# Kernel tuning notes

Measured on AMD Instinct MI355X. Metric: run time of the kernel, lower is better.

Reference implementation:

```python
import jax, jax.numpy as jnp
import numpy as np

E = 1024      # embed_dim
H = 16        # num_heads
HD = E // H   # head_dim = 64


def setup_inputs() -> dict:
    key = jax.random.key(0)
    ks = jax.random.split(key, 8)
    T, B, S = 1024, 4, 1024
    return {
        "query": jax.random.normal(ks[0], (T, B, E), jnp.float32),
        "key": jax.random.normal(ks[1], (S, B, E), jnp.float32),
        "value": jax.random.normal(ks[2], (S, B, E), jnp.float32),
        "attn_mask": jax.random.normal(ks[3], (T, S), jnp.float32),
        "key_padding_mask": jax.random.randint(ks[4], (B, S), 0, 2, jnp.int32),
        "in_proj_weight": jax.random.normal(ks[5], (3 * E, E), jnp.float32) * 0.02,
        "in_proj_bias": jnp.zeros((3 * E,), jnp.float32),
        "out_w": jax.random.normal(ks[6], (E, E), jnp.float32) * 0.02,
        "out_b": jnp.zeros((E,), jnp.float32),
    }


def reference(query, key, value, attn_mask, key_padding_mask,
              in_proj_weight, in_proj_bias, out_w, out_b):
    T, B, _ = query.shape
    S = key.shape[0]
    w_q, w_k, w_v = jnp.split(in_proj_weight, 3, axis=0)   # each [E, E]
    b_q, b_k, b_v = jnp.split(in_proj_bias, 3, axis=0)
    q = query @ w_q.T + b_q                                # [T, B, E]
    k = key @ w_k.T + b_k                                  # [S, B, E]
    v = value @ w_v.T + b_v                                # [S, B, E]
    # [len, B, E] -> [B*H, len, HD]
    q = q.reshape(T, B * H, HD).transpose(1, 0, 2) / jnp.sqrt(jnp.float32(HD))
    k = k.reshape(S, B * H, HD).transpose(1, 0, 2)
    v = v.reshape(S, B * H, HD).transpose(1, 0, 2)
    scores = jnp.einsum('bth,bsh->bts', q, k)              # [B*H, T, S]
    scores = scores + attn_mask[None]                      # float additive mask
    pad = key_padding_mask.astype(bool)                    # [B, S]
    pad = jnp.broadcast_to(pad[:, None, None, :], (B, H, 1, S)).reshape(B * H, 1, S)
    scores = jnp.where(pad, -jnp.inf, scores)
    weights = jax.nn.softmax(scores, axis=-1)              # dropout p=0 -> identity
    out = jnp.einsum('bts,bsh->bth', weights, v)           # [B*H, T, HD]
    out = out.transpose(1, 0, 2).reshape(T, B, E)
    out = out @ out_w.T + out_b
    weights_avg = weights.reshape(B, H, T, S).mean(axis=1) # sum/H == mean
    return out, weights_avg
```

## Files before the change

kernel.cpp:

```cpp
#include <hip/hip_runtime.h>
#include <stdint.h>

typedef short bf16x8 __attribute__((ext_vector_type(8)));
typedef float f32x4  __attribute__((ext_vector_type(4)));

#define LOG2E_F 1.4426950408889634f
#define QSCALE_F 0.1803368801111204f

__device__ __forceinline__ unsigned short f2bf(float f) {
    unsigned int u = __float_as_uint(f);
    return (unsigned short)((u + 0x7FFFu + ((u >> 16) & 1u)) >> 16);
}

__device__ __forceinline__ unsigned short f2bfu(float f) {
    return (unsigned short)((__float_as_uint(f) + 0x8000u) >> 16);
}

__device__ __forceinline__ uint4 pack8(float4 a, float4 b) {
    union { unsigned short us[8]; uint4 v; } p;
    p.us[0] = f2bf(a.x); p.us[1] = f2bf(a.y); p.us[2] = f2bf(a.z); p.us[3] = f2bf(a.w);
    p.us[4] = f2bf(b.x); p.us[5] = f2bf(b.y); p.us[6] = f2bf(b.z); p.us[7] = f2bf(b.w);
    return p.v;
}

__global__ __launch_bounds__(256)
void cvt_kernel(const float* __restrict__ q, const float* __restrict__ k,
                const float* __restrict__ v, const float* __restrict__ w,
                const float* __restrict__ ow,
                uint4* __restrict__ Xb, uint4* __restrict__ Wb, uint4* __restrict__ OWb)
{
    const unsigned g = blockIdx.x * 256 + threadIdx.x;
    const float* src;
    uint4* dst;
    if (g < 1572864u) {
        dst = Xb + g;
        if (g < 524288u)        src = q + (size_t)g * 8;
        else if (g < 1048576u)  src = k + (size_t)(g - 524288u) * 8;
        else                    src = v + (size_t)(g - 1048576u) * 8;
    } else if (g < 1966080u) {
        src = w + (size_t)(g - 1572864u) * 8;
        dst = Wb + (g - 1572864u);
    } else {
        src = ow + (size_t)(g - 1966080u) * 8;
        dst = OWb + (g - 1966080u);
    }
    float4 a = *(const float4*)src;
    float4 b = *(const float4*)(src + 4);
    *dst = pack8(a, b);
}

__global__ __launch_bounds__(256)
void qkv_proj_kernel(const unsigned short* __restrict__ Xb, const unsigned short* __restrict__ Wb,
                     const float* __restrict__ bias,
                     unsigned short* __restrict__ Qb, unsigned short* __restrict__ Kb,
                     unsigned short* __restrict__ Vtb)
{
    const int z = blockIdx.z;
    const int j   = blockIdx.x;
    const int xcd = j & 7, idx = j >> 3;
    const int row0 = ((xcd << 2) + (idx >> 3)) * 128;
    const int col0 = (idx & 7) * 128;
    const int wofs = z << 10;

    const unsigned short* A = Xb + (size_t)z * 4194304;
    const unsigned short* B = Wb;

    __shared__ __align__(16) unsigned short As[128 * 72];
    __shared__ __align__(16) unsigned short Bs[128 * 72];

    const int tid  = threadIdx.x;
    const int lane = tid & 63;
    const int wv   = tid >> 6;
    const int wr   = wv >> 1, wc = wv & 1;

    const f32x4 zero4 = {0.f, 0.f, 0.f, 0.f};
    f32x4 acc[4][4];
#pragma unroll
    for (int m = 0; m < 4; ++m)
#pragma unroll
        for (int n = 0; n < 4; ++n) acc[m][n] = zero4;

    const int srow = tid >> 1;
    const int scol = (tid & 1) << 5;
    const int arow = wr * 64 + (lane & 15);
    const int brow = wc * 64 + (lane & 15);
    const int kof  = (lane >> 4) << 3;

    const unsigned short* pa = A + (size_t)(row0 + srow) * 1024 + scol;
    const unsigned short* pb = B + (size_t)(wofs + col0 + srow) * 1024 + scol;
    uint4 ra0 = *(const uint4*)(pa + 0),  ra1 = *(const uint4*)(pa + 8);
    uint4 ra2 = *(const uint4*)(pa + 16), ra3 = *(const uint4*)(pa + 24);
    uint4 rb0 = *(const uint4*)(pb + 0),  rb1 = *(const uint4*)(pb + 8);
    uint4 rb2 = *(const uint4*)(pb + 16), rb3 = *(const uint4*)(pb + 24);

    for (int k0 = 0; k0 < 1024; k0 += 64) {
        __syncthreads();
        *(uint4*)&As[srow * 72 + scol]      = ra0;
        *(uint4*)&As[srow * 72 + scol + 8]  = ra1;
        *(uint4*)&As[srow * 72 + scol + 16] = ra2;
        *(uint4*)&As[srow * 72 + scol + 24] = ra3;
        *(uint4*)&Bs[srow * 72 + scol]      = rb0;
        *(uint4*)&Bs[srow * 72 + scol + 8]  = rb1;
        *(uint4*)&Bs[srow * 72 + scol + 16] = rb2;
        *(uint4*)&Bs[srow * 72 + scol + 24] = rb3;
        __syncthreads();

        if (k0 < 960) {
            pa = A + (size_t)(row0 + srow) * 1024 + k0 + 64 + scol;
            pb = B + (size_t)(wofs + col0 + srow) * 1024 + k0 + 64 + scol;
            ra0 = *(const uint4*)(pa + 0);  ra1 = *(const uint4*)(pa + 8);
            ra2 = *(const uint4*)(pa + 16); ra3 = *(const uint4*)(pa + 24);
            rb0 = *(const uint4*)(pb + 0);  rb1 = *(const uint4*)(pb + 8);
            rb2 = *(const uint4*)(pb + 16); rb3 = *(const uint4*)(pb + 24);
        }

#pragma unroll
        for (int kk = 0; kk < 2; ++kk) {
            bf16x8 af[4], bfr[4];
#pragma unroll
            for (int m = 0; m < 4; ++m)
                af[m] = *(const bf16x8*)&As[(arow + m * 16) * 72 + kk * 32 + kof];
#pragma unroll
            for (int n = 0; n < 4; ++n)
                bfr[n] = *(const bf16x8*)&Bs[(brow + n * 16) * 72 + kk * 32 + kof];
#pragma unroll
            for (int m = 0; m < 4; ++m)
#pragma unroll
                for (int n = 0; n < 4; ++n)
                    acc[m][n] = __builtin_amdgcn_mfma_f32_16x16x32_bf16(af[m], bfr[n], acc[m][n], 0, 0, 0);
        }
    }

    const int ccol = lane & 15;
    const int crow = (lane >> 4) << 2;
#pragma unroll
    for (int n = 0; n < 4; ++n) {
        const int gc   = col0 + wc * 64 + n * 16 + ccol;
        const float bv = bias[wofs + gc];
        const int head = gc >> 6, d = gc & 63;
#pragma unroll
        for (int m = 0; m < 4; ++m) {
#pragma unroll
            for (int r = 0; r < 4; ++r) {
                const int gr = row0 + wr * 64 + m * 16 + crow + r;
                const int t  = gr >> 2, b = gr & 3;
                const int bh = (b << 4) + head;
                float vv = acc[m][n][r] + bv;
                if (z == 0)      Qb [((size_t)bh << 16) + ((size_t)t << 6) + d]  = f2bf(vv * QSCALE_F);
                else if (z == 1) Kb [((size_t)bh << 16) + ((size_t)t << 6) + d]  = f2bf(vv);
                else             Vtb[((size_t)bh << 16) + ((size_t)d << 10) + t] = f2bf(vv);
            }
        }
    }
}

__global__ __launch_bounds__(512)
void flash_kernel(const unsigned short* __restrict__ Qb, const unsigned short* __restrict__ Kb,
                  const unsigned short* __restrict__ Vtb, const float* __restrict__ attn_mask,
                  const int* __restrict__ padmask,
                  float* __restrict__ rl_buf, unsigned short* __restrict__ attn_out)
{
    const int j   = blockIdx.x;
    const int xcd = j & 7, idx = j >> 3;
    const int bh  = xcd * 8 + (idx >> 3);
    const int t0  = (idx & 7) << 7;
    const int b   = bh >> 4, h = bh & 15;

    __shared__ __align__(16) unsigned short Ks[2][64 * 72];
    __shared__ __align__(16) unsigned short Vs[2][64 * 72];
    __shared__ __align__(16) unsigned short Ps[128 * 72];

    const int tid  = threadIdx.x;
    const int lane = tid & 63;
    const int wv   = tid >> 6;
    const int kof  = (lane >> 4) << 3;
    const int c16  = lane & 15;

    const unsigned short* Qbase = Qb  + ((size_t)bh << 16);
    const unsigned short* Kbase = Kb  + ((size_t)bh << 16);
    const unsigned short* Vbase = Vtb + ((size_t)bh << 16);

    bf16x8 qf[2];
#pragma unroll
    for (int kk = 0; kk < 2; ++kk)
        qf[kk] = *(const bf16x8*)(Qbase + ((size_t)(t0 + wv * 16 + c16) << 6) + kk * 32 + kof);

    const bf16x8 ones = {16256, 16256, 16256, 16256, 16256, 16256, 16256, 16256};

    const f32x4 zero4 = {0.f, 0.f, 0.f, 0.f};
    f32x4 acco[4];
#pragma unroll
    for (int nd = 0; nd < 4; ++nd) acco[nd] = zero4;
    f32x4 acc_l = zero4;

    const int srow_st = tid >> 3;
    const int scol_st = (tid & 7) << 3;

    const int rbase = wv * 16 + ((lane >> 4) << 2);
    const int tr    = t0 + rbase;

    const unsigned short* kp = Kbase + ((size_t)srow_st << 6) + scol_st;
    const unsigned short* vp = Vbase + ((size_t)srow_st << 10) + scol_st;
    uint4 ka = *(const uint4*)kp;
    uint4 kb = *(const uint4*)(kp + 4096);
    uint4 va = *(const uint4*)vp;
    uint4 vb = *(const uint4*)(vp + 64);

    for (int rd = 0; rd < 8; ++rd) {
        const int s0 = rd << 7;
        __syncthreads();
        *(uint4*)&Ks[0][srow_st * 72 + scol_st] = ka;
        *(uint4*)&Ks[1][srow_st * 72 + scol_st] = kb;
        *(uint4*)&Vs[0][srow_st * 72 + scol_st] = va;
        *(uint4*)&Vs[1][srow_st * 72 + scol_st] = vb;
        __syncthreads();

        if (rd < 7) {
            const int sn = s0 + 128;
            kp = Kbase + ((size_t)(sn + srow_st) << 6) + scol_st;
            vp = Vbase + ((size_t)srow_st << 10) + sn + scol_st;
            ka = *(const uint4*)kp;
            kb = *(const uint4*)(kp + 4096);
            va = *(const uint4*)vp;
            vb = *(const uint4*)(vp + 64);
        }

        f32x4 accsA[4], accsB[4];
#pragma unroll
        for (int n = 0; n < 4; ++n) { accsA[n] = zero4; accsB[n] = zero4; }
        __builtin_amdgcn_s_setprio(1);
#pragma unroll
        for (int n = 0; n < 4; ++n) {
            bf16x8 kfA0 = *(const bf16x8*)&Ks[0][(n * 16 + c16) * 72 + kof];
            bf16x8 kfA1 = *(const bf16x8*)&Ks[0][(n * 16 + c16) * 72 + 32 + kof];
            accsA[n] = __builtin_amdgcn_mfma_f32_16x16x32_bf16(qf[0], kfA0, accsA[n], 0, 0, 0);
            accsA[n] = __builtin_amdgcn_mfma_f32_16x16x32_bf16(qf[1], kfA1, accsA[n], 0, 0, 0);
            bf16x8 kfB0 = *(const bf16x8*)&Ks[1][(n * 16 + c16) * 72 + kof];
            bf16x8 kfB1 = *(const bf16x8*)&Ks[1][(n * 16 + c16) * 72 + 32 + kof];
            accsB[n] = __builtin_amdgcn_mfma_f32_16x16x32_bf16(qf[0], kfB0, accsB[n], 0, 0, 0);
            accsB[n] = __builtin_amdgcn_mfma_f32_16x16x32_bf16(qf[1], kfB1, accsB[n], 0, 0, 0);
        }
        __builtin_amdgcn_s_setprio(0);

        int padA[4], padB[4];
#pragma unroll
        for (int n = 0; n < 4; ++n) {
            padA[n] = padmask[(b << 10) + s0 + n * 16 + c16];
            padB[n] = padmask[(b << 10) + s0 + 64 + n * 16 + c16];
        }

#pragma unroll
        for (int r = 0; r < 4; ++r) {
            const float* mp = attn_mask + (size_t)(tr + r) * 1024 + s0 + c16;
            float x0 = fmaf(mp[ 0], LOG2E_F, accsA[0][r]);
            float x1 = fmaf(mp[16], LOG2E_F, accsA[1][r]);
            float x2 = fmaf(mp[32], LOG2E_F, accsA[2][r]);
            float x3 = fmaf(mp[48], LOG2E_F, accsA[3][r]);
            if (padA[0]) x0 = -1e30f;
            if (padA[1]) x1 = -1e30f;
            if (padA[2]) x2 = -1e30f;
            if (padA[3]) x3 = -1e30f;
            const int prow = rbase + r;
            Ps[prow * 72 +  0 + c16] = f2bfu(__builtin_amdgcn_exp2f(x0));
            Ps[prow * 72 + 16 + c16] = f2bfu(__builtin_amdgcn_exp2f(x1));
            Ps[prow * 72 + 32 + c16] = f2bfu(__builtin_amdgcn_exp2f(x2));
            Ps[prow * 72 + 48 + c16] = f2bfu(__builtin_amdgcn_exp2f(x3));
        }
        __builtin_amdgcn_s_setprio(1);
#pragma unroll
        for (int kk2 = 0; kk2 < 2; ++kk2) {
            bf16x8 pf = *(const bf16x8*)&Ps[(wv * 16 + c16) * 72 + kk2 * 32 + kof];
#pragma unroll
            for (int nd = 0; nd < 4; ++nd) {
                bf16x8 vf = *(const bf16x8*)&Vs[0][(nd * 16 + c16) * 72 + kk2 * 32 + kof];
                acco[nd] = __builtin_amdgcn_mfma_f32_16x16x32_bf16(pf, vf, acco[nd], 0, 0, 0);
            }
            acc_l = __builtin_amdgcn_mfma_f32_16x16x32_bf16(pf, ones, acc_l, 0, 0, 0);
        }
        __builtin_amdgcn_s_setprio(0);

#pragma unroll
        for (int r = 0; r < 4; ++r) {
            const float* mp = attn_mask + (size_t)(tr + r) * 1024 + s0 + 64 + c16;
            float x0 = fmaf(mp[ 0], LOG2E_F, accsB[0][r]);
            float x1 = fmaf(mp[16], LOG2E_F, accsB[1][r]);
            float x2 = fmaf(mp[32], LOG2E_F, accsB[2][r]);
            float x3 = fmaf(mp[48], LOG2E_F, accsB[3][r]);
            if (padB[0]) x0 = -1e30f;
            if (padB[1]) x1 = -1e30f;
            if (padB[2]) x2 = -1e30f;
            if (padB[3]) x3 = -1e30f;
            const int prow = rbase + r;
            Ps[prow * 72 +  0 + c16] = f2bfu(__builtin_amdgcn_exp2f(x0));
            Ps[prow * 72 + 16 + c16] = f2bfu(__builtin_amdgcn_exp2f(x1));
            Ps[prow * 72 + 32 + c16] = f2bfu(__builtin_amdgcn_exp2f(x2));
            Ps[prow * 72 + 48 + c16] = f2bfu(__builtin_amdgcn_exp2f(x3));
        }
        __builtin_amdgcn_s_setprio(1);
#pragma unroll
        for (int kk2 = 0; kk2 < 2; ++kk2) {
            bf16x8 pf = *(const bf16x8*)&Ps[(wv * 16 + c16) * 72 + kk2 * 32 + kof];
#pragma unroll
            for (int nd = 0; nd < 4; ++nd) {
                bf16x8 vf = *(const bf16x8*)&Vs[1][(nd * 16 + c16) * 72 + kk2 * 32 + kof];
                acco[nd] = __builtin_amdgcn_mfma_f32_16x16x32_bf16(pf, vf, acco[nd], 0, 0, 0);
            }
            acc_l = __builtin_amdgcn_mfma_f32_16x16x32_bf16(pf, ones, acc_l, 0, 0, 0);
        }
        __builtin_amdgcn_s_setprio(0);
    }

#pragma unroll
    for (int r = 0; r < 4; ++r) {
        const int t = t0 + rbase + r;
        const float rl = 1.0f / acc_l[r];
        if (c16 == 0)
            rl_buf[(bh << 10) + t] = rl;
#pragma unroll
        for (int nd = 0; nd < 4; ++nd) {
            const int d = nd * 16 + c16;
            attn_out[((size_t)t * 4 + b) * 1024 + h * 64 + d] = f2bf(acco[nd][r] * rl);
        }
    }
}

__global__ __launch_bounds__(256)
void wavg_kernel(const unsigned short* __restrict__ Qb, const unsigned short* __restrict__ Kb,
                 const float* __restrict__ attn_mask, const int* __restrict__ padmask,
                 const float* __restrict__ rl_buf, float* __restrict__ wout)
{
    const int j   = blockIdx.x;
    const int xcd = j & 7;
    const int b   = xcd >> 1;
    const int rr  = ((j >> 3) << 1) + (xcd & 1);
    const int t0  = (rr >> 4) << 6;
    const int s0  = (rr & 15) << 6;

    __shared__ __align__(16) unsigned short Qs[64 * 72];
    __shared__ __align__(16) unsigned short Ks2[64 * 72];

    const int tid  = threadIdx.x;
    const int lane = tid & 63;
    const int wv   = tid >> 6;
    const int wr   = wv >> 1, wc = wv & 1;
    const int kof  = (lane >> 4) << 3;
    const int srow_st = tid >> 2;
    const int scol_st = (tid & 3) << 4;

    const int t_base = t0 + wr * 32 + ((lane >> 4) << 2);
    const int s_base = s0 + wc * 32 + (lane & 15);

    int pad2[2];
#pragma unroll
    for (int nn = 0; nn < 2; ++nn) pad2[nn] = padmask[(b << 10) + s_base + nn * 16];

    float maskv[2][2][4];
#pragma unroll
    for (int mm = 0; mm < 2; ++mm)
#pragma unroll
        for (int r = 0; r < 4; ++r)
#pragma unroll
            for (int nn = 0; nn < 2; ++nn)
                maskv[mm][nn][r] = attn_mask[(size_t)(t_base + mm * 16 + r) * 1024 + s_base + nn * 16] * LOG2E_F;

    float wsum[2][2][4];
#pragma unroll
    for (int mm = 0; mm < 2; ++mm)
#pragma unroll
        for (int nn = 0; nn < 2; ++nn)
#pragma unroll
            for (int r = 0; r < 4; ++r) wsum[mm][nn][r] = 0.f;

    for (int h = 0; h < 16; ++h) {
        const int bh = (b << 4) + h;
        __syncthreads();
        {
            const unsigned short* qp = Qb + ((size_t)bh << 16) + ((size_t)(t0 + srow_st) << 6) + scol_st;
            *(uint4*)&Qs[srow_st * 72 + scol_st]     = *(const uint4*)qp;
            *(uint4*)&Qs[srow_st * 72 + scol_st + 8] = *(const uint4*)(qp + 8);
            const unsigned short* kp = Kb + ((size_t)bh << 16) + ((size_t)(s0 + srow_st) << 6) + scol_st;
            *(uint4*)&Ks2[srow_st * 72 + scol_st]     = *(const uint4*)kp;
            *(uint4*)&Ks2[srow_st * 72 + scol_st + 8] = *(const uint4*)(kp + 8);
        }
        __syncthreads();

        float rlv[2][4];
#pragma unroll
        for (int mm = 0; mm < 2; ++mm)
#pragma unroll
            for (int r = 0; r < 4; ++r)
                rlv[mm][r] = rl_buf[(bh << 10) + t_base + mm * 16 + r];

        const f32x4 zero4 = {0.f, 0.f, 0.f, 0.f};
        f32x4 accs[2][2];
#pragma unroll
        for (int mm = 0; mm < 2; ++mm)
#pragma unroll
            for (int nn = 0; nn < 2; ++nn) accs[mm][nn] = zero4;
#pragma unroll
        for (int nn = 0; nn < 2; ++nn) {
            bf16x8 kf0 = *(const bf16x8*)&Ks2[(wc * 32 + nn * 16 + (lane & 15)) * 72 + kof];
            bf16x8 kf1 = *(const bf16x8*)&Ks2[(wc * 32 + nn * 16 + (lane & 15)) * 72 + 32 + kof];
#pragma unroll
            for (int mm = 0; mm < 2; ++mm) {
                bf16x8 qf0 = *(const bf16x8*)&Qs[(wr * 32 + mm * 16 + (lane & 15)) * 72 + kof];
                bf16x8 qf1 = *(const bf16x8*)&Qs[(wr * 32 + mm * 16 + (lane & 15)) * 72 + 32 + kof];
                accs[mm][nn] = __builtin_amdgcn_mfma_f32_16x16x32_bf16(qf0, kf0, accs[mm][nn], 0, 0, 0);
                accs[mm][nn] = __builtin_amdgcn_mfma_f32_16x16x32_bf16(qf1, kf1, accs[mm][nn], 0, 0, 0);
            }
        }
#pragma unroll
        for (int mm = 0; mm < 2; ++mm)
#pragma unroll
            for (int nn = 0; nn < 2; ++nn)
#pragma unroll
                for (int r = 0; r < 4; ++r)
                    if (!pad2[nn]) {
                        float x = accs[mm][nn][r] + maskv[mm][nn][r];
                        wsum[mm][nn][r] += __builtin_amdgcn_exp2f(x) * rlv[mm][r];
                    }
    }

#pragma unroll
    for (int mm = 0; mm < 2; ++mm)
#pragma unroll
        for (int nn = 0; nn < 2; ++nn)
#pragma unroll
            for (int r = 0; r < 4; ++r)
                wout[((size_t)b << 20) + (size_t)(t_base + mm * 16 + r) * 1024 + s_base + nn * 16]
                    = wsum[mm][nn][r] * 0.0625f;
}

__global__ __launch_bounds__(256)
void out_proj_kernel(const unsigned short* __restrict__ A, const unsigned short* __restrict__ Wb,
                     const float* __restrict__ bias, float* __restrict__ out)
{
    const int j   = blockIdx.x;
    const int xcd = j & 7, idx = j >> 3;
    const int row0 = ((xcd << 2) + (idx >> 3)) * 128;
    const int col0 = (idx & 7) * 128;

    __shared__ __align__(16) unsigned short As[128 * 72];
    __shared__ __align__(16) unsigned short Bs[128 * 72];

    const int tid  = threadIdx.x;
    const int lane = tid & 63;
    const int wv   = tid >> 6;
    const int wr   = wv >> 1, wc = wv & 1;

    const f32x4 zero4 = {0.f, 0.f, 0.f, 0.f};
    f32x4 acc[4][4];
#pragma unroll
    for (int m = 0; m < 4; ++m)
#pragma unroll
        for (int n = 0; n < 4; ++n) acc[m][n] = zero4;

    const int srow = tid >> 1;
    const int scol = (tid & 1) << 5;
    const int arow = wr * 64 + (lane & 15);
    const int brow = wc * 64 + (lane & 15);
    const int kof  = (lane >> 4) << 3;

    const unsigned short* pa = A  + (size_t)(row0 + srow) * 1024 + scol;
    const unsigned short* pb = Wb + (size_t)(col0 + srow) * 1024 + scol;
    uint4 ra0 = *(const uint4*)(pa + 0),  ra1 = *(const uint4*)(pa + 8);
    uint4 ra2 = *(const uint4*)(pa + 16), ra3 = *(const uint4*)(pa + 24);
    uint4 rb0 = *(const uint4*)(pb + 0),  rb1 = *(const uint4*)(pb + 8);
    uint4 rb2 = *(const uint4*)(pb + 16), rb3 = *(const uint4*)(pb + 24);

    for (int k0 = 0; k0 < 1024; k0 += 64) {
        __syncthreads();
        *(uint4*)&As[srow * 72 + scol]      = ra0;
        *(uint4*)&As[srow * 72 + scol + 8]  = ra1;
        *(uint4*)&As[srow * 72 + scol + 16] = ra2;
        *(uint4*)&As[srow * 72 + scol + 24] = ra3;
        *(uint4*)&Bs[srow * 72 + scol]      = rb0;
        *(uint4*)&Bs[srow * 72 + scol + 8]  = rb1;
        *(uint4*)&Bs[srow * 72 + scol + 16] = rb2;
        *(uint4*)&Bs[srow * 72 + scol + 24] = rb3;
        __syncthreads();

        if (k0 < 960) {
            pa = A  + (size_t)(row0 + srow) * 1024 + k0 + 64 + scol;
            pb = Wb + (size_t)(col0 + srow) * 1024 + k0 + 64 + scol;
            ra0 = *(const uint4*)(pa + 0);  ra1 = *(const uint4*)(pa + 8);
            ra2 = *(const uint4*)(pa + 16); ra3 = *(const uint4*)(pa + 24);
            rb0 = *(const uint4*)(pb + 0);  rb1 = *(const uint4*)(pb + 8);
            rb2 = *(const uint4*)(pb + 16); rb3 = *(const uint4*)(pb + 24);
        }

#pragma unroll
        for (int kk = 0; kk < 2; ++kk) {
            bf16x8 af[4], bfr[4];
#pragma unroll
            for (int m = 0; m < 4; ++m)
                af[m] = *(const bf16x8*)&As[(arow + m * 16) * 72 + kk * 32 + kof];
#pragma unroll
            for (int n = 0; n < 4; ++n)
                bfr[n] = *(const bf16x8*)&Bs[(brow + n * 16) * 72 + kk * 32 + kof];
#pragma unroll
            for (int m = 0; m < 4; ++m)
#pragma unroll
                for (int n = 0; n < 4; ++n)
                    acc[m][n] = __builtin_amdgcn_mfma_f32_16x16x32_bf16(af[m], bfr[n], acc[m][n], 0, 0, 0);
        }
    }

    const int ccol = lane & 15;
    const int crow = (lane >> 4) << 2;
#pragma unroll
    for (int n = 0; n < 4; ++n) {
        const int gc   = col0 + wc * 64 + n * 16 + ccol;
        const float bv = bias[gc];
#pragma unroll
        for (int m = 0; m < 4; ++m) {
#pragma unroll
            for (int r = 0; r < 4; ++r) {
                const int gr = row0 + wr * 64 + m * 16 + crow + r;
                out[(size_t)gr * 1024 + gc] = acc[m][n][r] + bv;
            }
        }
    }
}

extern "C" void kernel_launch(void* const* d_in, const int* in_sizes, int n_in,
                              void* d_out, int out_size, void* d_ws, size_t ws_size,
                              hipStream_t stream)
{
    const float* query     = (const float*)d_in[0];
    const float* key       = (const float*)d_in[1];
    const float* value     = (const float*)d_in[2];
    const float* attn_mask = (const float*)d_in[3];
    const int*   padmask   = (const int*)  d_in[4];
    const float* in_proj_w = (const float*)d_in[5];
    const float* in_proj_b = (const float*)d_in[6];
    const float* out_w     = (const float*)d_in[7];
    const float* out_b     = (const float*)d_in[8];

    float* out  = (float*)d_out;
    float* wavg = out + 4194304;

    char* ws = (char*)d_ws;
    unsigned short* Qb     = (unsigned short*)(ws);
    unsigned short* Kb     = (unsigned short*)(ws + 8388608);
    unsigned short* Vtb    = (unsigned short*)(ws + 16777216);
    unsigned short* Xb     = (unsigned short*)(ws + 25165824);
    unsigned short* attn_o = (unsigned short*)(ws + 25165824);
    unsigned short* Wb     = (unsigned short*)(ws + 50331648);
    unsigned short* OWb    = (unsigned short*)(ws + 56623104);
    float*          rl_buf = (float*)(ws + 58720256);

    cvt_kernel<<<dim3(8192), 256, 0, stream>>>(query, key, value, in_proj_w, out_w,
                                               (uint4*)Xb, (uint4*)Wb, (uint4*)OWb);
    qkv_proj_kernel<<<dim3(256, 1, 3), 256, 0, stream>>>(Xb, Wb, in_proj_b, Qb, Kb, Vtb);
    flash_kernel<<<dim3(512), 512, 0, stream>>>(Qb, Kb, Vtb, attn_mask, padmask,
                                                rl_buf, attn_o);
    wavg_kernel<<<dim3(1024), 256, 0, stream>>>(Qb, Kb, attn_mask, padmask,
                                                rl_buf, wavg);
    out_proj_kernel<<<dim3(256), 256, 0, stream>>>(attn_o, OWb, out_b, out);
}
```

Measured before the change: 151.9 us.

## Double-buffer shared-memory K/V and Q/K tiles in flash and weights kernels

Both the flash attention kernel and the averaged-weights kernel now keep two shared-memory buffers for their K/V (or Q/K) tiles. The next tile is written into the alternate buffer while the current one is consumed, and global loads are prefetched two iterations ahead. This cuts the two barriers per iteration down to one and gives global load latency more time to hide. In exchange it doubles LDS use in both kernels, which may lower occupancy, and it keeps more prefetch registers live.

```diff
diff --git a/kernel.cpp b/kernel.cpp
--- a/kernel.cpp
+++ b/kernel.cpp
@@ -166,8 +166,8 @@
     const int t0  = (idx & 7) << 7;
     const int b   = bh >> 4, h = bh & 15;
 
-    __shared__ __align__(16) unsigned short Ks[2][64 * 72];
-    __shared__ __align__(16) unsigned short Vs[2][64 * 72];
+    __shared__ __align__(16) unsigned short Ks[2][2][64 * 72];
+    __shared__ __align__(16) unsigned short Vs[2][2][64 * 72];
     __shared__ __align__(16) unsigned short Ps[128 * 72];
 
     const int tid  = threadIdx.x;
@@ -201,46 +201,43 @@
 
     const unsigned short* kp = Kbase + ((size_t)srow_st << 6) + scol_st;
     const unsigned short* vp = Vbase + ((size_t)srow_st << 10) + scol_st;
-    uint4 ka = *(const uint4*)kp;
-    uint4 kb = *(const uint4*)(kp + 4096);
-    uint4 va = *(const uint4*)vp;
-    uint4 vb = *(const uint4*)(vp + 64);
+    uint4 kA = *(const uint4*)kp;
+    uint4 kB = *(const uint4*)(kp + 4096);
+    uint4 vA = *(const uint4*)vp;
+    uint4 vB = *(const uint4*)(vp + 64);
+
+    *(uint4*)&Ks[0][0][srow_st * 72 + scol_st] = kA;
+    *(uint4*)&Ks[0][1][srow_st * 72 + scol_st] = kB;
+    *(uint4*)&Vs[0][0][srow_st * 72 + scol_st] = vA;
+    *(uint4*)&Vs[0][1][srow_st * 72 + scol_st] = vB;
+
+    kp = Kbase + ((size_t)(128 + srow_st) << 6) + scol_st;
+    vp = Vbase + ((size_t)srow_st << 10) + 128 + scol_st;
+    kA = *(const uint4*)kp;
+    kB = *(const uint4*)(kp + 4096);
+    vA = *(const uint4*)vp;
+    vB = *(const uint4*)(vp + 64);
+    __syncthreads();
 
     for (int rd = 0; rd < 8; ++rd) {
-        const int s0 = rd << 7;
-        __syncthreads();
-        *(uint4*)&Ks[0][srow_st * 72 + scol_st] = ka;
-        *(uint4*)&Ks[1][srow_st * 72 + scol_st] = kb;
-        *(uint4*)&Vs[0][srow_st * 72 + scol_st] = va;
-        *(uint4*)&Vs[1][srow_st * 72 + scol_st] = vb;
-        __syncthreads();
+        const int cur = rd & 1;
+        const int s0  = rd << 7;
 
         if (rd < 7) {
-            const int sn = s0 + 128;
+            *(uint4*)&Ks[cur ^ 1][0][srow_st * 72 + scol_st] = kA;
+            *(uint4*)&Ks[cur ^ 1][1][srow_st * 72 + scol_st] = kB;
+            *(uint4*)&Vs[cur ^ 1][0][srow_st * 72 + scol_st] = vA;
+            *(uint4*)&Vs[cur ^ 1][1][srow_st * 72 + scol_st] = vB;
+        }
+        if (rd < 6) {
+            const int sn = s0 + 256;
             kp = Kbase + ((size_t)(sn + srow_st) << 6) + scol_st;
             vp = Vbase + ((size_t)srow_st << 10) + sn + scol_st;
-            ka = *(const uint4*)kp;
-            kb = *(const uint4*)(kp + 4096);
-            va = *(const uint4*)vp;
-            vb = *(const uint4*)(vp + 64);
-        }
-
-        f32x4 accsA[4], accsB[4];
-#pragma unroll
-        for (int n = 0; n < 4; ++n) { accsA[n] = zero4; accsB[n] = zero4; }
-        __builtin_amdgcn_s_setprio(1);
-#pragma unroll
-        for (int n = 0; n < 4; ++n) {
-            bf16x8 kfA0 = *(const bf16x8*)&Ks[0][(n * 16 + c16) * 72 + kof];
-            bf16x8 kfA1 = *(const bf16x8*)&Ks[0][(n * 16 + c16) * 72 + 32 + kof];
-            accsA[n] = __builtin_amdgcn_mfma_f32_16x16x32_bf16(qf[0], kfA0, accsA[n], 0, 0, 0);
-            accsA[n] = __builtin_amdgcn_mfma_f32_16x16x32_bf16(qf[1], kfA1, accsA[n], 0, 0, 0);
-            bf16x8 kfB0 = *(const bf16x8*)&Ks[1][(n * 16 + c16) * 72 + kof];
-            bf16x8 kfB1 = *(const bf16x8*)&Ks[1][(n * 16 + c16) * 72 + 32 + kof];
-            accsB[n] = __builtin_amdgcn_mfma_f32_16x16x32_bf16(qf[0], kfB0, accsB[n], 0, 0, 0);
-            accsB[n] = __builtin_amdgcn_mfma_f32_16x16x32_bf16(qf[1], kfB1, accsB[n], 0, 0, 0);
-        }
-        __builtin_amdgcn_s_setprio(0);
+            kA = *(const uint4*)kp;
+            kB = *(const uint4*)(kp + 4096);
+            vA = *(const uint4*)vp;
+            vB = *(const uint4*)(vp + 64);
+        }
 
         int padA[4], padB[4];
 #pragma unroll
@@ -248,6 +245,23 @@
             padA[n] = padmask[(b << 10) + s0 + n * 16 + c16];
             padB[n] = padmask[(b << 10) + s0 + 64 + n * 16 + c16];
         }
+
+        f32x4 accsA[4], accsB[4];
+#pragma unroll
+        for (int n = 0; n < 4; ++n) { accsA[n] = zero4; accsB[n] = zero4; }
+        __builtin_amdgcn_s_setprio(1);
+#pragma unroll
+        for (int n = 0; n < 4; ++n) {
+            bf16x8 kfA0 = *(const bf16x8*)&Ks[cur][0][(n * 16 + c16) * 72 + kof];
+            bf16x8 kfA1 = *(const bf16x8*)&Ks[cur][0][(n * 16 + c16) * 72 + 32 + kof];
+            accsA[n] = __builtin_amdgcn_mfma_f32_16x16x32_bf16(qf[0], kfA0, accsA[n], 0, 0, 0);
+            accsA[n] = __builtin_amdgcn_mfma_f32_16x16x32_bf16(qf[1], kfA1, accsA[n], 0, 0, 0);
+            bf16x8 kfB0 = *(const bf16x8*)&Ks[cur][1][(n * 16 + c16) * 72 + kof];
+            bf16x8 kfB1 = *(const bf16x8*)&Ks[cur][1][(n * 16 + c16) * 72 + 32 + kof];
+            accsB[n] = __builtin_amdgcn_mfma_f32_16x16x32_bf16(qf[0], kfB0, accsB[n], 0, 0, 0);
+            accsB[n] = __builtin_amdgcn_mfma_f32_16x16x32_bf16(qf[1], kfB1, accsB[n], 0, 0, 0);
+        }
+        __builtin_amdgcn_s_setprio(0);
 
 #pragma unroll
         for (int r = 0; r < 4; ++r) {
@@ -272,7 +286,7 @@
             bf16x8 pf = *(const bf16x8*)&Ps[(wv * 16 + c16) * 72 + kk2 * 32 + kof];
 #pragma unroll
             for (int nd = 0; nd < 4; ++nd) {
-                bf16x8 vf = *(const bf16x8*)&Vs[0][(nd * 16 + c16) * 72 + kk2 * 32 + kof];
+                bf16x8 vf = *(const bf16x8*)&Vs[cur][0][(nd * 16 + c16) * 72 + kk2 * 32 + kof];
                 acco[nd] = __builtin_amdgcn_mfma_f32_16x16x32_bf16(pf, vf, acco[nd], 0, 0, 0);
             }
             acc_l = __builtin_amdgcn_mfma_f32_16x16x32_bf16(pf, ones, acc_l, 0, 0, 0);
@@ -302,12 +316,14 @@
             bf16x8 pf = *(const bf16x8*)&Ps[(wv * 16 + c16) * 72 + kk2 * 32 + kof];
 #pragma unroll
             for (int nd = 0; nd < 4; ++nd) {
-                bf16x8 vf = *(const bf16x8*)&Vs[1][(nd * 16 + c16) * 72 + kk2 * 32 + kof];
+                bf16x8 vf = *(const bf16x8*)&Vs[cur][1][(nd * 16 + c16) * 72 + kk2 * 32 + kof];
                 acco[nd] = __builtin_amdgcn_mfma_f32_16x16x32_bf16(pf, vf, acco[nd], 0, 0, 0);
             }
             acc_l = __builtin_amdgcn_mfma_f32_16x16x32_bf16(pf, ones, acc_l, 0, 0, 0);
         }
         __builtin_amdgcn_s_setprio(0);
+
+        if (rd < 7) __syncthreads();
     }
 
 #pragma unroll
@@ -336,8 +352,8 @@
     const int t0  = (rr >> 4) << 6;
     const int s0  = (rr & 15) << 6;
 
-    __shared__ __align__(16) unsigned short Qs[64 * 72];
-    __shared__ __align__(16) unsigned short Ks2[64 * 72];
+    __shared__ __align__(16) unsigned short Qs[2][64 * 72];
+    __shared__ __align__(16) unsigned short Ks2[2][64 * 72];
 
     const int tid  = threadIdx.x;
     const int lane = tid & 63;
@@ -371,18 +387,42 @@
 #pragma unroll
             for (int r = 0; r < 4; ++r) wsum[mm][nn][r] = 0.f;
 
+    const unsigned short* qsrc = Qb + ((size_t)(t0 + srow_st) << 6) + scol_st;
+    const unsigned short* ksrc = Kb + ((size_t)(s0 + srow_st) << 6) + scol_st;
+    const size_t bh0 = (size_t)(b << 4) << 16;
+
+    uint4 q0 = *(const uint4*)(qsrc + bh0);
+    uint4 q1 = *(const uint4*)(qsrc + bh0 + 8);
+    uint4 k0 = *(const uint4*)(ksrc + bh0);
+    uint4 k1 = *(const uint4*)(ksrc + bh0 + 8);
+    *(uint4*)&Qs[0][srow_st * 72 + scol_st]      = q0;
+    *(uint4*)&Qs[0][srow_st * 72 + scol_st + 8]  = q1;
+    *(uint4*)&Ks2[0][srow_st * 72 + scol_st]     = k0;
+    *(uint4*)&Ks2[0][srow_st * 72 + scol_st + 8] = k1;
+    q0 = *(const uint4*)(qsrc + bh0 + 65536);
+    q1 = *(const uint4*)(qsrc + bh0 + 65536 + 8);
+    k0 = *(const uint4*)(ksrc + bh0 + 65536);
+    k1 = *(const uint4*)(ksrc + bh0 + 65536 + 8);
+    __syncthreads();
+
+#pragma unroll 2
     for (int h = 0; h < 16; ++h) {
-        const int bh = (b << 4) + h;
-        __syncthreads();
-        {
-            const unsigned short* qp = Qb + ((size_t)bh << 16) + ((size_t)(t0 + srow_st) << 6) + scol_st;
-            *(uint4*)&Qs[srow_st * 72 + scol_st]     = *(const uint4*)qp;
-            *(uint4*)&Qs[srow_st * 72 + scol_st + 8] = *(const uint4*)(qp + 8);
-            const unsigned short* kp = Kb + ((size_t)bh << 16) + ((size_t)(s0 + srow_st) << 6) + scol_st;
-            *(uint4*)&Ks2[srow_st * 72 + scol_st]     = *(const uint4*)kp;
-            *(uint4*)&Ks2[srow_st * 72 + scol_st + 8] = *(const uint4*)(kp + 8);
-        }
-        __syncthreads();
+        const int cur = h & 1;
+        const int bh  = (b << 4) + h;
+
+        if (h < 15) {
+            *(uint4*)&Qs[cur ^ 1][srow_st * 72 + scol_st]      = q0;
+            *(uint4*)&Qs[cur ^ 1][srow_st * 72 + scol_st + 8]  = q1;
+            *(uint4*)&Ks2[cur ^ 1][srow_st * 72 + scol_st]     = k0;
+            *(uint4*)&Ks2[cur ^ 1][srow_st * 72 + scol_st + 8] = k1;
+        }
+        if (h < 14) {
+            const size_t of = bh0 + (size_t)(h + 2) * 65536;
+            q0 = *(const uint4*)(qsrc + of);
+            q1 = *(const uint4*)(qsrc + of + 8);
+            k0 = *(const uint4*)(ksrc + of);
+            k1 = *(const uint4*)(ksrc + of + 8);
+        }
 
         float rlv[2][4];
 #pragma unroll
@@ -399,12 +439,12 @@
             for (int nn = 0; nn < 2; ++nn) accs[mm][nn] = zero4;
 #pragma unroll
         for (int nn = 0; nn < 2; ++nn) {
-            bf16x8 kf0 = *(const bf16x8*)&Ks2[(wc * 32 + nn * 16 + (lane & 15)) * 72 + kof];
-            bf16x8 kf1 = *(const bf16x8*)&Ks2[(wc * 32 + nn * 16 + (lane & 15)) * 72 + 32 + kof];
+            bf16x8 kf0 = *(const bf16x8*)&Ks2[cur][(wc * 32 + nn * 16 + (lane & 15)) * 72 + kof];
+            bf16x8 kf1 = *(const bf16x8*)&Ks2[cur][(wc * 32 + nn * 16 + (lane & 15)) * 72 + 32 + kof];
 #pragma unroll
             for (int mm = 0; mm < 2; ++mm) {
-                bf16x8 qf0 = *(const bf16x8*)&Qs[(wr * 32 + mm * 16 + (lane & 15)) * 72 + kof];
-                bf16x8 qf1 = *(const bf16x8*)&Qs[(wr * 32 + mm * 16 + (lane & 15)) * 72 + 32 + kof];
+                bf16x8 qf0 = *(const bf16x8*)&Qs[cur][(wr * 32 + mm * 16 + (lane & 15)) * 72 + kof];
+                bf16x8 qf1 = *(const bf16x8*)&Qs[cur][(wr * 32 + mm * 16 + (lane & 15)) * 72 + 32 + kof];
                 accs[mm][nn] = __builtin_amdgcn_mfma_f32_16x16x32_bf16(qf0, kf0, accs[mm][nn], 0, 0, 0);
                 accs[mm][nn] = __builtin_amdgcn_mfma_f32_16x16x32_bf16(qf1, kf1, accs[mm][nn], 0, 0, 0);
             }
@@ -419,6 +459,8 @@
                         float x = accs[mm][nn][r] + maskv[mm][nn][r];
                         wsum[mm][nn][r] += __builtin_amdgcn_exp2f(x) * rlv[mm][r];
                     }
+
+        if (h < 15) __syncthreads();
     }
 
 #pragma unroll
```

After: 151.2 us. About the same (-0.5%).
